# Kernel tuning notes

Hardware: AMD Instinct MI355X
Metric: run time of the kernel (lower is better)

## Reference

```python
import jax, jax.numpy as jnp
import numpy as np

NB_VARS = 2_000_000
N0 = 2 + 2 * NB_VARS      # input vector length: [zero, one, pos0, neg0, pos1, neg1, ...]
M0 = 4_000_000            # prod layer 0 outputs (binary fan-in)
M1 = 1_000_000            # sum  layer 1 outputs (irregular fan-in)
M2 = 500_000              # prod layer 2 outputs (binary fan-in)
M3 = 125_000              # sum  layer 3 outputs (irregular fan-in)


def setup_inputs() -> dict:
    key = jax.random.key(0)
    ks = jax.random.split(key, 7)
    x_pos = jax.random.uniform(ks[0], (NB_VARS,), dtype=jnp.float32)
    ix_in0 = jax.random.randint(ks[1], (2 * M0,), 0, N0)            # edges of prod layer 0
    ix_in1 = jax.random.randint(ks[2], (8_000_000,), 0, M0)         # edges of sum layer 1
    ix_out1 = jnp.sort(jax.random.randint(ks[3], (8_000_000,), 0, M1))
    ix_in2 = jax.random.randint(ks[4], (2 * M2,), 0, M1)            # edges of prod layer 2
    ix_in3 = jax.random.randint(ks[5], (1_000_000,), 0, M2)         # edges of sum layer 3
    ix_out3 = jnp.sort(jax.random.randint(ks[6], (1_000_000,), 0, M3))
    return {"x_pos": x_pos, "ix_in0": ix_in0, "ix_in1": ix_in1, "ix_out1": ix_out1,
            "ix_in2": ix_in2, "ix_in3": ix_in3, "ix_out3": ix_out3}


def reference(x_pos, ix_in0, ix_in1, ix_out1, ix_in2, ix_in3, ix_out3):
    # encode_input (real semiring): neg = negate(pos) = 1 - pos; interleave; prepend [zero=0, one=1]
    neg = 1.0 - x_pos
    units = jnp.array([0.0, 1.0], dtype=x_pos.dtype)
    x = jnp.concatenate([units, jnp.stack([x_pos, neg], axis=1).reshape(-1)])  # [N0]

    # layer 0: product layer, binary fan-in -> gather + pairwise multiply
    e0 = x[ix_in0].reshape(M0, 2)
    x = e0[:, 0] * e0[:, 1]                                                    # [M0]

    # layer 1: sum layer, irregular fan-in -> gather + segment-sum
    x = jax.ops.segment_sum(x[ix_in1], ix_out1, num_segments=M1)               # [M1]

    # layer 2: product layer, binary fan-in
    e2 = x[ix_in2].reshape(M2, 2)
    x = e2[:, 0] * e2[:, 1]                                                    # [M2]

    # layer 3: sum layer, irregular fan-in
    x = jax.ops.segment_sum(x[ix_in3], ix_out3, num_segments=M3)               # [M3]
    return x
```

## Files before the change

kernel.cpp:

```cpp
#include <hip/hip_runtime.h>
#include <hip/hip_fp16.h>


#define PERS_BLOCKS 2048
#define PERS_THREADS 256
#define WBITS_H 20

typedef __attribute__((ext_vector_type(4))) int   iv4;
typedef __attribute__((ext_vector_type(4))) float fv4;
typedef __attribute__((ext_vector_type(4))) unsigned int uv4;

__device__ __forceinline__ iv4 nt_load4(const int* p) {
    return __builtin_nontemporal_load((const iv4*)p);
}

__global__ void init_kernel(const float* __restrict__ in, unsigned int* __restrict__ x16,
                            float* __restrict__ y1, float* __restrict__ out,
                            int n4, int nz1, int nzo) {
    int t = blockIdx.x * blockDim.x + threadIdx.x;
    if (t < n4) {
        fv4 f = __builtin_nontemporal_load((const fv4*)(in + 4 * (size_t)t));
        __half2 lo = __floats2half2_rn(f.x, f.y);
        __half2 hi = __floats2half2_rn(f.z, f.w);
        unsigned int rlo = *(const unsigned int*)&lo;
        unsigned int rhi = *(const unsigned int*)&hi;
        x16[2 * t]     = rlo;
        x16[2 * t + 1] = rhi;
    }
    if (t < nz1) {
        fv4 z = {0.f, 0.f, 0.f, 0.f};
        __builtin_nontemporal_store(z, (fv4*)(y1 + 4 * (size_t)t));
    }
    if (t < nzo) {
        fv4 z = {0.f, 0.f, 0.f, 0.f};
        __builtin_nontemporal_store(z, (fv4*)(out + 4 * (size_t)t));
    }
}

__device__ __forceinline__ float decode16(const __half* __restrict__ xp, int idx) {
    int k = (idx - 2) >> 1;
    k = k < 0 ? 0 : k;
    float v = __half2float(xp[k]);
    v = (idx & 1) ? 1.0f - v : v;
    if (idx < 2) v = (float)idx;
    return v;
}

__global__ void layer0_prod8_kernel(const __half* __restrict__ x16,
                                    const int* __restrict__ ix,
                                    unsigned int* __restrict__ out16, int nT) {
    int t = blockIdx.x * blockDim.x + threadIdx.x;
    if (t >= nT) return;
    iv4 p0 = nt_load4(ix + 16 * (size_t)t);
    iv4 p1 = nt_load4(ix + 16 * (size_t)t + 4);
    iv4 p2 = nt_load4(ix + 16 * (size_t)t + 8);
    iv4 p3 = nt_load4(ix + 16 * (size_t)t + 12);
    float a0 = decode16(x16, p0.x), b0 = decode16(x16, p0.y);
    float a1 = decode16(x16, p0.z), b1 = decode16(x16, p0.w);
    float a2 = decode16(x16, p1.x), b2 = decode16(x16, p1.y);
    float a3 = decode16(x16, p1.z), b3 = decode16(x16, p1.w);
    float a4 = decode16(x16, p2.x), b4 = decode16(x16, p2.y);
    float a5 = decode16(x16, p2.z), b5 = decode16(x16, p2.w);
    float a6 = decode16(x16, p3.x), b6 = decode16(x16, p3.y);
    float a7 = decode16(x16, p3.z), b7 = decode16(x16, p3.w);
    __half2 h0 = __floats2half2_rn(a0 * b0, a1 * b1);
    __half2 h1 = __floats2half2_rn(a2 * b2, a3 * b3);
    __half2 h2 = __floats2half2_rn(a4 * b4, a5 * b5);
    __half2 h3 = __floats2half2_rn(a6 * b6, a7 * b7);
    uv4 r;
    r.x = *(const unsigned int*)&h0;
    r.y = *(const unsigned int*)&h1;
    r.z = *(const unsigned int*)&h2;
    r.w = *(const unsigned int*)&h3;
    __builtin_nontemporal_store(r, (uv4*)(out16 + 4 * (size_t)t));
}

template<int NS, int NWIN>
__global__ __launch_bounds__(PERS_THREADS)
void sum_win_h_kernel(const __half* __restrict__ vin,
                      const int* __restrict__ ix_in,
                      const int* __restrict__ ix_out,
                      float* __restrict__ out, int nT4) {
    const int nTh  = gridDim.x * blockDim.x;
    const int gtid = blockIdx.x * blockDim.x + threadIdx.x;
    const int lane = threadIdx.x & 63;

    iv4    a[NS];
    iv4    sg[NS];
    float4 v[NS];
    bool   act[NS];
    #pragma unroll
    for (int s = 0; s < NS; ++s) {
        int t = s * nTh + gtid;
        act[s] = (t < nT4);
        if (act[s]) {
            a[s]  = nt_load4(ix_in  + 4 * (size_t)t);
            sg[s] = nt_load4(ix_out + 4 * (size_t)t);
        } else {
            a[s]  = (iv4){-1, -1, -1, -1};
            sg[s] = (iv4){-1, -1, -1, -1};
        }
        v[s] = make_float4(0.f, 0.f, 0.f, 0.f);
    }

    #pragma unroll
    for (int w = 0; w < NWIN; ++w) {
        #pragma unroll
        for (int s = 0; s < NS; ++s) {
            if ((a[s].x >> WBITS_H) == w) v[s].x = __half2float(vin[a[s].x]);
            if ((a[s].y >> WBITS_H) == w) v[s].y = __half2float(vin[a[s].y]);
            if ((a[s].z >> WBITS_H) == w) v[s].z = __half2float(vin[a[s].z]);
            if ((a[s].w >> WBITS_H) == w) v[s].w = __half2float(vin[a[s].w]);
        }
    }

    #pragma unroll
    for (int s = 0; s < NS; ++s) {
        int seg = -1; float val = 0.f;
        if (act[s]) {
            int cur = sg[s].x; float acc = v[s].x;
            if (sg[s].y == cur) acc += v[s].y; else { atomicAdd(&out[cur], acc); cur = sg[s].y; acc = v[s].y; }
            if (sg[s].z == cur) acc += v[s].z; else { atomicAdd(&out[cur], acc); cur = sg[s].z; acc = v[s].z; }
            if (sg[s].w == cur) acc += v[s].w; else { atomicAdd(&out[cur], acc); cur = sg[s].w; acc = v[s].w; }
            seg = cur; val = acc;
        }
        #pragma unroll
        for (int off = 1; off < 64; off <<= 1) {
            float vv = __shfl_up(val, off, 64);
            int   ss = __shfl_up(seg, off, 64);
            if (lane >= off && ss == seg) val += vv;
        }
        int seg_next = __shfl_down(seg, 1, 64);
        bool is_last = (lane == 63) || (seg_next != seg);
        if (act[s] && is_last) atomicAdd(&out[seg], val);
    }
}

__global__ void sum4_f32_kernel(const float* __restrict__ vin,
                                const int* __restrict__ ix_in,
                                const int* __restrict__ ix_out,
                                float* __restrict__ out, int nT4) {
    int t = blockIdx.x * blockDim.x + threadIdx.x;
    int lane = threadIdx.x & 63;
    int seg = -1; float val = 0.f;
    if (t < nT4) {
        iv4 a  = nt_load4(ix_in  + 4 * (size_t)t);
        iv4 sg = nt_load4(ix_out + 4 * (size_t)t);
        float v0 = vin[a.x], v1 = vin[a.y], v2 = vin[a.z], v3 = vin[a.w];
        int cur = sg.x; float acc = v0;
        if (sg.y == cur) acc += v1; else { atomicAdd(&out[cur], acc); cur = sg.y; acc = v1; }
        if (sg.z == cur) acc += v2; else { atomicAdd(&out[cur], acc); cur = sg.z; acc = v2; }
        if (sg.w == cur) acc += v3; else { atomicAdd(&out[cur], acc); cur = sg.w; acc = v3; }
        seg = cur; val = acc;
    }
    #pragma unroll
    for (int off = 1; off < 64; off <<= 1) {
        float vv = __shfl_up(val, off, 64);
        int   ss = __shfl_up(seg, off, 64);
        if (lane >= off && ss == seg) val += vv;
    }
    int seg_next = __shfl_down(seg, 1, 64);
    bool is_last = (lane == 63) || (seg_next != seg);
    if (t < nT4 && is_last) atomicAdd(&out[seg], val);
}

__global__ void prod2_kernel(const float* __restrict__ vin,
                             const int* __restrict__ ix,
                             float2* __restrict__ out, int nT) {
    int t = blockIdx.x * blockDim.x + threadIdx.x;
    if (t >= nT) return;
    iv4 p = nt_load4(ix + 4 * (size_t)t);
    float a0 = vin[p.x], b0 = vin[p.y];
    float a1 = vin[p.z], b1 = vin[p.w];
    float2 r; r.x = a0 * b0; r.y = a1 * b1;
    out[t] = r;
}

extern "C" void kernel_launch(void* const* d_in, const int* in_sizes, int n_in,
                              void* d_out, int out_size, void* d_ws, size_t ws_size,
                              hipStream_t stream) {
    const float* x_pos  = (const float*)d_in[0];
    const int*   ix_in0 = (const int*)d_in[1];
    const int*   ix_in1 = (const int*)d_in[2];
    const int*   ix_out1= (const int*)d_in[3];
    const int*   ix_in2 = (const int*)d_in[4];
    const int*   ix_in3 = (const int*)d_in[5];
    const int*   ix_out3= (const int*)d_in[6];
    float* out = (float*)d_out;

    const int NV = in_sizes[0];
    const int M0 = in_sizes[1] / 2;
    const int E1 = in_sizes[2];
    const int M1 = 1000000;
    const int M2 = in_sizes[4] / 2;
    const int E3 = in_sizes[5];
    const int M3 = out_size;

    char* ws = (char*)d_ws;
    __half* y0  = (__half*)(ws);
    float*  y1  = (float*)(ws + (size_t)8  * 1024 * 1024);
    float*  y2  = (float*)(ws + (size_t)12 * 1024 * 1024);
    __half* x16 = (__half*)(ws + (size_t)14 * 1024 * 1024);

    const int B = 256;

    int n4  = NV / 4;
    int nz1 = M1 / 4;
    int nzo = M3 / 4;
    init_kernel<<<(n4 + B - 1) / B, B, 0, stream>>>(
        x_pos, (unsigned int*)x16, y1, out, n4, nz1, nzo);

    int t0 = M0 / 8;
    layer0_prod8_kernel<<<(t0 + B - 1) / B, B, 0, stream>>>(
        x16, ix_in0, (unsigned int*)y0, t0);

    int t1 = E1 / 4;
    sum_win_h_kernel<4, 4><<<PERS_BLOCKS, PERS_THREADS, 0, stream>>>(
        y0, ix_in1, ix_out1, y1, t1);

    int t2 = M2 / 2;
    prod2_kernel<<<(t2 + B - 1) / B, B, 0, stream>>>(
        y1, ix_in2, (float2*)y2, t2);

    int t3 = E3 / 4;
    sum4_f32_kernel<<<(t3 + B - 1) / B, B, 0, stream>>>(
        y2, ix_in3, ix_out3, out, t3);
}
```

Measured before the change: 253.8 us.

## Replace atomics with plain stores for wave-interior segments; restructure layer0 striding

In both segment-sum kernels, a segment whose run lies entirely inside one wavefront is now written with a plain store instead of an atomicAdd. Shuffles of the neighbouring lanes' first and last segment IDs decide this, and any segment that might span a wave boundary still uses atomics. The goal is to cut atomic traffic to global memory. Layer 0 is also rewritten so each thread handles four strided pairs-of-pairs, which changes the load pattern from 64-byte per-thread chunks to coalesced 16-byte loads.

```diff
diff --git a/kernel.cpp b/kernel.cpp
--- a/kernel.cpp
+++ b/kernel.cpp
@@ -46,33 +46,30 @@
     return v;
 }
 
-__global__ void layer0_prod8_kernel(const __half* __restrict__ x16,
-                                    const int* __restrict__ ix,
-                                    unsigned int* __restrict__ out16, int nT) {
-    int t = blockIdx.x * blockDim.x + threadIdx.x;
-    if (t >= nT) return;
-    iv4 p0 = nt_load4(ix + 16 * (size_t)t);
-    iv4 p1 = nt_load4(ix + 16 * (size_t)t + 4);
-    iv4 p2 = nt_load4(ix + 16 * (size_t)t + 8);
-    iv4 p3 = nt_load4(ix + 16 * (size_t)t + 12);
-    float a0 = decode16(x16, p0.x), b0 = decode16(x16, p0.y);
-    float a1 = decode16(x16, p0.z), b1 = decode16(x16, p0.w);
-    float a2 = decode16(x16, p1.x), b2 = decode16(x16, p1.y);
-    float a3 = decode16(x16, p1.z), b3 = decode16(x16, p1.w);
-    float a4 = decode16(x16, p2.x), b4 = decode16(x16, p2.y);
-    float a5 = decode16(x16, p2.z), b5 = decode16(x16, p2.w);
-    float a6 = decode16(x16, p3.x), b6 = decode16(x16, p3.y);
-    float a7 = decode16(x16, p3.z), b7 = decode16(x16, p3.w);
-    __half2 h0 = __floats2half2_rn(a0 * b0, a1 * b1);
-    __half2 h1 = __floats2half2_rn(a2 * b2, a3 * b3);
-    __half2 h2 = __floats2half2_rn(a4 * b4, a5 * b5);
-    __half2 h3 = __floats2half2_rn(a6 * b6, a7 * b7);
-    uv4 r;
-    r.x = *(const unsigned int*)&h0;
-    r.y = *(const unsigned int*)&h1;
-    r.z = *(const unsigned int*)&h2;
-    r.w = *(const unsigned int*)&h3;
-    __builtin_nontemporal_store(r, (uv4*)(out16 + 4 * (size_t)t));
+#define NS0 4
+__global__ void layer0_prod_kernel(const __half* __restrict__ x16,
+                                   const int* __restrict__ ix,
+                                   unsigned int* __restrict__ out16, int nQ) {
+    const int nTh  = gridDim.x * blockDim.x;
+    const int gtid = blockIdx.x * blockDim.x + threadIdx.x;
+    #pragma unroll
+    for (int s = 0; s < NS0; ++s) {
+        int t = s * nTh + gtid;
+        if (t < nQ) {
+            iv4 p = nt_load4(ix + 4 * (size_t)t);
+            float a0 = decode16(x16, p.x), b0 = decode16(x16, p.y);
+            float a1 = decode16(x16, p.z), b1 = decode16(x16, p.w);
+            __half2 h = __floats2half2_rn(a0 * b0, a1 * b1);
+            __builtin_nontemporal_store(*(const unsigned int*)&h, out16 + (size_t)t);
+        }
+    }
+}
+
+__device__ __forceinline__ void flush_run(float* __restrict__ out, int cur, float acc,
+                                          bool first, int lane, int prvw) {
+    bool plain = first ? (lane > 0 && prvw != cur) : true;
+    if (plain) out[cur] = acc;
+    else atomicAdd(&out[cur], acc);
 }
 
 template<int NS, int NWIN>
@@ -116,12 +113,22 @@
 
     #pragma unroll
     for (int s = 0; s < NS; ++s) {
+        int seg_first = __shfl(sg[s].x, 0, 64);
+        int prvw      = __shfl_up(sg[s].w, 1, 64);
+        int nxt_first = __shfl_down(sg[s].x, 1, 64);
+
         int seg = -1; float val = 0.f;
         if (act[s]) {
-            int cur = sg[s].x; float acc = v[s].x;
-            if (sg[s].y == cur) acc += v[s].y; else { atomicAdd(&out[cur], acc); cur = sg[s].y; acc = v[s].y; }
-            if (sg[s].z == cur) acc += v[s].z; else { atomicAdd(&out[cur], acc); cur = sg[s].z; acc = v[s].z; }
-            if (sg[s].w == cur) acc += v[s].w; else { atomicAdd(&out[cur], acc); cur = sg[s].w; acc = v[s].w; }
+            int cur = sg[s].x; float acc = v[s].x; bool first = true;
+            if (sg[s].y == cur) acc += v[s].y;
+            else { flush_run(out, cur, acc, first, lane, prvw);
+                   cur = sg[s].y; acc = v[s].y; first = false; }
+            if (sg[s].z == cur) acc += v[s].z;
+            else { flush_run(out, cur, acc, first, lane, prvw);
+                   cur = sg[s].z; acc = v[s].z; first = false; }
+            if (sg[s].w == cur) acc += v[s].w;
+            else { flush_run(out, cur, acc, first, lane, prvw);
+                   cur = sg[s].w; acc = v[s].w; first = false; }
             seg = cur; val = acc;
         }
         #pragma unroll
@@ -132,7 +139,11 @@
         }
         int seg_next = __shfl_down(seg, 1, 64);
         bool is_last = (lane == 63) || (seg_next != seg);
-        if (act[s] && is_last) atomicAdd(&out[seg], val);
+        bool cont    = (lane == 63) || (nxt_first == seg);
+        if (act[s] && is_last) {
+            if (!cont && seg > seg_first) out[seg] = val;
+            else atomicAdd(&out[seg], val);
+        }
     }
 }
 
@@ -142,15 +153,32 @@
                                 float* __restrict__ out, int nT4) {
     int t = blockIdx.x * blockDim.x + threadIdx.x;
     int lane = threadIdx.x & 63;
+    bool act = (t < nT4);
+    iv4 a, sg;
+    if (act) {
+        a  = nt_load4(ix_in  + 4 * (size_t)t);
+        sg = nt_load4(ix_out + 4 * (size_t)t);
+    } else {
+        a  = (iv4){-1, -1, -1, -1};
+        sg = (iv4){-1, -1, -1, -1};
+    }
+    int seg_first = __shfl(sg.x, 0, 64);
+    int prvw      = __shfl_up(sg.w, 1, 64);
+    int nxt_first = __shfl_down(sg.x, 1, 64);
+
     int seg = -1; float val = 0.f;
-    if (t < nT4) {
-        iv4 a  = nt_load4(ix_in  + 4 * (size_t)t);
-        iv4 sg = nt_load4(ix_out + 4 * (size_t)t);
+    if (act) {
         float v0 = vin[a.x], v1 = vin[a.y], v2 = vin[a.z], v3 = vin[a.w];
-        int cur = sg.x; float acc = v0;
-        if (sg.y == cur) acc += v1; else { atomicAdd(&out[cur], acc); cur = sg.y; acc = v1; }
-        if (sg.z == cur) acc += v2; else { atomicAdd(&out[cur], acc); cur = sg.z; acc = v2; }
-        if (sg.w == cur) acc += v3; else { atomicAdd(&out[cur], acc); cur = sg.w; acc = v3; }
+        int cur = sg.x; float acc = v0; bool first = true;
+        if (sg.y == cur) acc += v1;
+        else { flush_run(out, cur, acc, first, lane, prvw);
+               cur = sg.y; acc = v1; first = false; }
+        if (sg.z == cur) acc += v2;
+        else { flush_run(out, cur, acc, first, lane, prvw);
+               cur = sg.z; acc = v2; first = false; }
+        if (sg.w == cur) acc += v3;
+        else { flush_run(out, cur, acc, first, lane, prvw);
+               cur = sg.w; acc = v3; first = false; }
         seg = cur; val = acc;
     }
     #pragma unroll
@@ -161,7 +189,11 @@
     }
     int seg_next = __shfl_down(seg, 1, 64);
     bool is_last = (lane == 63) || (seg_next != seg);
-    if (t < nT4 && is_last) atomicAdd(&out[seg], val);
+    bool cont    = (lane == 63) || (nxt_first == seg);
+    if (act && is_last) {
+        if (!cont && seg > seg_first) out[seg] = val;
+        else atomicAdd(&out[seg], val);
+    }
 }
 
 __global__ void prod2_kernel(const float* __restrict__ vin,
@@ -210,9 +242,10 @@
     init_kernel<<<(n4 + B - 1) / B, B, 0, stream>>>(
         x_pos, (unsigned int*)x16, y1, out, n4, nz1, nzo);
 
-    int t0 = M0 / 8;
-    layer0_prod8_kernel<<<(t0 + B - 1) / B, B, 0, stream>>>(
-        x16, ix_in0, (unsigned int*)y0, t0);
+    int nQ = M0 / 2;
+    int g0 = (nQ + NS0 * B - 1) / (NS0 * B);
+    layer0_prod_kernel<<<g0, B, 0, stream>>>(
+        x16, ix_in0, (unsigned int*)y0, nQ);
 
     int t1 = E1 / 4;
     sum_win_h_kernel<4, 4><<<PERS_BLOCKS, PERS_THREADS, 0, stream>>>(
```

Measured after the change: 282.2 us. +11.2%, slower.

## Replace windowed persistent layer-1 gather with simple one-pass grid kernel

Applied to the files above, without the earlier changes.

Removes the persistent kernel that split the fp16 gather into four address windows, with four work items per thread, to keep each window cache-resident. Uses a plain one-thread-per-4-edges kernel over the whole grid, gathering all four values directly before the segmented reduction. This drops the windowing loop and its per-window compare overhead and raises parallelism, but gives up the L2 locality the windows were meant to provide for the 8 MB fp16 source.

```diff
diff --git a/kernel.cpp b/kernel.cpp
--- a/kernel.cpp
+++ b/kernel.cpp
@@ -1,10 +1,6 @@
 #include <hip/hip_runtime.h>
 #include <hip/hip_fp16.h>
 
-
-#define PERS_BLOCKS 2048
-#define PERS_THREADS 256
-#define WBITS_H 20
 
 typedef __attribute__((ext_vector_type(4))) int   iv4;
 typedef __attribute__((ext_vector_type(4))) float fv4;
@@ -75,65 +71,35 @@
     __builtin_nontemporal_store(r, (uv4*)(out16 + 4 * (size_t)t));
 }
 
-template<int NS, int NWIN>
-__global__ __launch_bounds__(PERS_THREADS)
-void sum_win_h_kernel(const __half* __restrict__ vin,
-                      const int* __restrict__ ix_in,
-                      const int* __restrict__ ix_out,
-                      float* __restrict__ out, int nT4) {
-    const int nTh  = gridDim.x * blockDim.x;
-    const int gtid = blockIdx.x * blockDim.x + threadIdx.x;
-    const int lane = threadIdx.x & 63;
-
-    iv4    a[NS];
-    iv4    sg[NS];
-    float4 v[NS];
-    bool   act[NS];
+__global__ void sum4_h_kernel(const __half* __restrict__ vin,
+                              const int* __restrict__ ix_in,
+                              const int* __restrict__ ix_out,
+                              float* __restrict__ out, int nT4) {
+    int t = blockIdx.x * blockDim.x + threadIdx.x;
+    int lane = threadIdx.x & 63;
+    int seg = -1; float val = 0.f;
+    if (t < nT4) {
+        iv4 a  = nt_load4(ix_in  + 4 * (size_t)t);
+        iv4 sg = nt_load4(ix_out + 4 * (size_t)t);
+        float v0 = __half2float(vin[a.x]);
+        float v1 = __half2float(vin[a.y]);
+        float v2 = __half2float(vin[a.z]);
+        float v3 = __half2float(vin[a.w]);
+        int cur = sg.x; float acc = v0;
+        if (sg.y == cur) acc += v1; else { atomicAdd(&out[cur], acc); cur = sg.y; acc = v1; }
+        if (sg.z == cur) acc += v2; else { atomicAdd(&out[cur], acc); cur = sg.z; acc = v2; }
+        if (sg.w == cur) acc += v3; else { atomicAdd(&out[cur], acc); cur = sg.w; acc = v3; }
+        seg = cur; val = acc;
+    }
     #pragma unroll
-    for (int s = 0; s < NS; ++s) {
-        int t = s * nTh + gtid;
-        act[s] = (t < nT4);
-        if (act[s]) {
-            a[s]  = nt_load4(ix_in  + 4 * (size_t)t);
-            sg[s] = nt_load4(ix_out + 4 * (size_t)t);
-        } else {
-            a[s]  = (iv4){-1, -1, -1, -1};
-            sg[s] = (iv4){-1, -1, -1, -1};
-        }
-        v[s] = make_float4(0.f, 0.f, 0.f, 0.f);
+    for (int off = 1; off < 64; off <<= 1) {
+        float vv = __shfl_up(val, off, 64);
+        int   ss = __shfl_up(seg, off, 64);
+        if (lane >= off && ss == seg) val += vv;
     }
-
-    #pragma unroll
-    for (int w = 0; w < NWIN; ++w) {
-        #pragma unroll
-        for (int s = 0; s < NS; ++s) {
-            if ((a[s].x >> WBITS_H) == w) v[s].x = __half2float(vin[a[s].x]);
-            if ((a[s].y >> WBITS_H) == w) v[s].y = __half2float(vin[a[s].y]);
-            if ((a[s].z >> WBITS_H) == w) v[s].z = __half2float(vin[a[s].z]);
-            if ((a[s].w >> WBITS_H) == w) v[s].w = __half2float(vin[a[s].w]);
-        }
-    }
-
-    #pragma unroll
-    for (int s = 0; s < NS; ++s) {
-        int seg = -1; float val = 0.f;
-        if (act[s]) {
-            int cur = sg[s].x; float acc = v[s].x;
-            if (sg[s].y == cur) acc += v[s].y; else { atomicAdd(&out[cur], acc); cur = sg[s].y; acc = v[s].y; }
-            if (sg[s].z == cur) acc += v[s].z; else { atomicAdd(&out[cur], acc); cur = sg[s].z; acc = v[s].z; }
-            if (sg[s].w == cur) acc += v[s].w; else { atomicAdd(&out[cur], acc); cur = sg[s].w; acc = v[s].w; }
-            seg = cur; val = acc;
-        }
-        #pragma unroll
-        for (int off = 1; off < 64; off <<= 1) {
-            float vv = __shfl_up(val, off, 64);
-            int   ss = __shfl_up(seg, off, 64);
-            if (lane >= off && ss == seg) val += vv;
-        }
-        int seg_next = __shfl_down(seg, 1, 64);
-        bool is_last = (lane == 63) || (seg_next != seg);
-        if (act[s] && is_last) atomicAdd(&out[seg], val);
-    }
+    int seg_next = __shfl_down(seg, 1, 64);
+    bool is_last = (lane == 63) || (seg_next != seg);
+    if (t < nT4 && is_last) atomicAdd(&out[seg], val);
 }
 
 __global__ void sum4_f32_kernel(const float* __restrict__ vin,
@@ -215,7 +181,7 @@
         x16, ix_in0, (unsigned int*)y0, t0);
 
     int t1 = E1 / 4;
-    sum_win_h_kernel<4, 4><<<PERS_BLOCKS, PERS_THREADS, 0, stream>>>(
+    sum4_h_kernel<<<(t1 + B - 1) / B, B, 0, stream>>>(
         y0, ix_in1, ix_out1, y1, t1);
 
     int t2 = M2 / 2;
```

New measurement: 266.2 us. 4.9% more time.

## Fuse input encoding and zeroing into layer 0, fold layer-2 product into layer 3

Applied to the files above, without the earlier changes.

Removes the separate init kernel by decoding fp32 inputs directly in the layer-0 gather and zeroing the accumulation buffers there. Removes the layer-2 product kernel by having the layer-3 segment-sum gather the index pair and multiply on the fly. This cuts two launches and the intermediate buffer traffic. In exchange, layer 3 does redundant gathers for reused nodes, and the layer-0 gather reads a larger fp32 table with worse cache locality.

```diff
diff --git a/kernel.cpp b/kernel.cpp
--- a/kernel.cpp
+++ b/kernel.cpp
@@ -14,55 +14,43 @@
     return __builtin_nontemporal_load((const iv4*)p);
 }
 
-__global__ void init_kernel(const float* __restrict__ in, unsigned int* __restrict__ x16,
-                            float* __restrict__ y1, float* __restrict__ out,
-                            int n4, int nz1, int nzo) {
+__device__ __forceinline__ float decode32(const float* __restrict__ xp, int idx) {
+    int k = (idx - 2) >> 1;
+    k = k < 0 ? 0 : k;
+    float v = xp[k];
+    v = (idx & 1) ? 1.0f - v : v;
+    if (idx < 2) v = (float)idx;
+    return v;
+}
+
+__global__ void layer0_prod8_zero_kernel(const float* __restrict__ xp,
+                                         const int* __restrict__ ix,
+                                         unsigned int* __restrict__ out16,
+                                         float* __restrict__ y1,
+                                         float* __restrict__ outv,
+                                         int nT, int nz1, int nzo) {
     int t = blockIdx.x * blockDim.x + threadIdx.x;
-    if (t < n4) {
-        fv4 f = __builtin_nontemporal_load((const fv4*)(in + 4 * (size_t)t));
-        __half2 lo = __floats2half2_rn(f.x, f.y);
-        __half2 hi = __floats2half2_rn(f.z, f.w);
-        unsigned int rlo = *(const unsigned int*)&lo;
-        unsigned int rhi = *(const unsigned int*)&hi;
-        x16[2 * t]     = rlo;
-        x16[2 * t + 1] = rhi;
-    }
     if (t < nz1) {
         fv4 z = {0.f, 0.f, 0.f, 0.f};
         __builtin_nontemporal_store(z, (fv4*)(y1 + 4 * (size_t)t));
     }
     if (t < nzo) {
         fv4 z = {0.f, 0.f, 0.f, 0.f};
-        __builtin_nontemporal_store(z, (fv4*)(out + 4 * (size_t)t));
-    }
-}
-
-__device__ __forceinline__ float decode16(const __half* __restrict__ xp, int idx) {
-    int k = (idx - 2) >> 1;
-    k = k < 0 ? 0 : k;
-    float v = __half2float(xp[k]);
-    v = (idx & 1) ? 1.0f - v : v;
-    if (idx < 2) v = (float)idx;
-    return v;
-}
-
-__global__ void layer0_prod8_kernel(const __half* __restrict__ x16,
-                                    const int* __restrict__ ix,
-                                    unsigned int* __restrict__ out16, int nT) {
-    int t = blockIdx.x * blockDim.x + threadIdx.x;
+        __builtin_nontemporal_store(z, (fv4*)(outv + 4 * (size_t)t));
+    }
     if (t >= nT) return;
     iv4 p0 = nt_load4(ix + 16 * (size_t)t);
     iv4 p1 = nt_load4(ix + 16 * (size_t)t + 4);
     iv4 p2 = nt_load4(ix + 16 * (size_t)t + 8);
     iv4 p3 = nt_load4(ix + 16 * (size_t)t + 12);
-    float a0 = decode16(x16, p0.x), b0 = decode16(x16, p0.y);
-    float a1 = decode16(x16, p0.z), b1 = decode16(x16, p0.w);
-    float a2 = decode16(x16, p1.x), b2 = decode16(x16, p1.y);
-    float a3 = decode16(x16, p1.z), b3 = decode16(x16, p1.w);
-    float a4 = decode16(x16, p2.x), b4 = decode16(x16, p2.y);
-    float a5 = decode16(x16, p2.z), b5 = decode16(x16, p2.w);
-    float a6 = decode16(x16, p3.x), b6 = decode16(x16, p3.y);
-    float a7 = decode16(x16, p3.z), b7 = decode16(x16, p3.w);
+    float a0 = decode32(xp, p0.x), b0 = decode32(xp, p0.y);
+    float a1 = decode32(xp, p0.z), b1 = decode32(xp, p0.w);
+    float a2 = decode32(xp, p1.x), b2 = decode32(xp, p1.y);
+    float a3 = decode32(xp, p1.z), b3 = decode32(xp, p1.w);
+    float a4 = decode32(xp, p2.x), b4 = decode32(xp, p2.y);
+    float a5 = decode32(xp, p2.z), b5 = decode32(xp, p2.w);
+    float a6 = decode32(xp, p3.x), b6 = decode32(xp, p3.y);
+    float a7 = decode32(xp, p3.z), b7 = decode32(xp, p3.w);
     __half2 h0 = __floats2half2_rn(a0 * b0, a1 * b1);
     __half2 h1 = __floats2half2_rn(a2 * b2, a3 * b3);
     __half2 h2 = __floats2half2_rn(a4 * b4, a5 * b5);
@@ -136,17 +124,25 @@
     }
 }
 
-__global__ void sum4_f32_kernel(const float* __restrict__ vin,
-                                const int* __restrict__ ix_in,
-                                const int* __restrict__ ix_out,
-                                float* __restrict__ out, int nT4) {
+__global__ void sum4_prod_f32_kernel(const float* __restrict__ y1,
+                                     const int* __restrict__ ix2,
+                                     const int* __restrict__ ix_in3,
+                                     const int* __restrict__ ix_out3,
+                                     float* __restrict__ out, int nT4) {
     int t = blockIdx.x * blockDim.x + threadIdx.x;
     int lane = threadIdx.x & 63;
     int seg = -1; float val = 0.f;
     if (t < nT4) {
-        iv4 a  = nt_load4(ix_in  + 4 * (size_t)t);
-        iv4 sg = nt_load4(ix_out + 4 * (size_t)t);
-        float v0 = vin[a.x], v1 = vin[a.y], v2 = vin[a.z], v3 = vin[a.w];
+        iv4 a  = nt_load4(ix_in3  + 4 * (size_t)t);
+        iv4 sg = nt_load4(ix_out3 + 4 * (size_t)t);
+        int2 q0 = *(const int2*)(ix2 + 2 * (size_t)a.x);
+        int2 q1 = *(const int2*)(ix2 + 2 * (size_t)a.y);
+        int2 q2 = *(const int2*)(ix2 + 2 * (size_t)a.z);
+        int2 q3 = *(const int2*)(ix2 + 2 * (size_t)a.w);
+        float v0 = y1[q0.x] * y1[q0.y];
+        float v1 = y1[q1.x] * y1[q1.y];
+        float v2 = y1[q2.x] * y1[q2.y];
+        float v3 = y1[q3.x] * y1[q3.y];
         int cur = sg.x; float acc = v0;
         if (sg.y == cur) acc += v1; else { atomicAdd(&out[cur], acc); cur = sg.y; acc = v1; }
         if (sg.z == cur) acc += v2; else { atomicAdd(&out[cur], acc); cur = sg.z; acc = v2; }
@@ -162,18 +158,6 @@
     int seg_next = __shfl_down(seg, 1, 64);
     bool is_last = (lane == 63) || (seg_next != seg);
     if (t < nT4 && is_last) atomicAdd(&out[seg], val);
-}
-
-__global__ void prod2_kernel(const float* __restrict__ vin,
-                             const int* __restrict__ ix,
-                             float2* __restrict__ out, int nT) {
-    int t = blockIdx.x * blockDim.x + threadIdx.x;
-    if (t >= nT) return;
-    iv4 p = nt_load4(ix + 4 * (size_t)t);
-    float a0 = vin[p.x], b0 = vin[p.y];
-    float a1 = vin[p.z], b1 = vin[p.w];
-    float2 r; r.x = a0 * b0; r.y = a1 * b1;
-    out[t] = r;
 }
 
 extern "C" void kernel_launch(void* const* d_in, const int* in_sizes, int n_in,
@@ -188,41 +172,29 @@
     const int*   ix_out3= (const int*)d_in[6];
     float* out = (float*)d_out;
 
-    const int NV = in_sizes[0];
     const int M0 = in_sizes[1] / 2;
     const int E1 = in_sizes[2];
     const int M1 = 1000000;
-    const int M2 = in_sizes[4] / 2;
     const int E3 = in_sizes[5];
     const int M3 = out_size;
 
     char* ws = (char*)d_ws;
-    __half* y0  = (__half*)(ws);
-    float*  y1  = (float*)(ws + (size_t)8  * 1024 * 1024);
-    float*  y2  = (float*)(ws + (size_t)12 * 1024 * 1024);
-    __half* x16 = (__half*)(ws + (size_t)14 * 1024 * 1024);
+    __half* y0 = (__half*)(ws);
+    float*  y1 = (float*)(ws + (size_t)8 * 1024 * 1024);
 
     const int B = 256;
 
-    int n4  = NV / 4;
+    int t0  = M0 / 8;
     int nz1 = M1 / 4;
     int nzo = M3 / 4;
-    init_kernel<<<(n4 + B - 1) / B, B, 0, stream>>>(
-        x_pos, (unsigned int*)x16, y1, out, n4, nz1, nzo);
-
-    int t0 = M0 / 8;
-    layer0_prod8_kernel<<<(t0 + B - 1) / B, B, 0, stream>>>(
-        x16, ix_in0, (unsigned int*)y0, t0);
+    layer0_prod8_zero_kernel<<<(t0 + B - 1) / B, B, 0, stream>>>(
+        x_pos, ix_in0, (unsigned int*)y0, y1, out, t0, nz1, nzo);
 
     int t1 = E1 / 4;
     sum_win_h_kernel<4, 4><<<PERS_BLOCKS, PERS_THREADS, 0, stream>>>(
         y0, ix_in1, ix_out1, y1, t1);
 
-    int t2 = M2 / 2;
-    prod2_kernel<<<(t2 + B - 1) / B, B, 0, stream>>>(
-        y1, ix_in2, (float2*)y2, t2);
-
     int t3 = E3 / 4;
-    sum4_f32_kernel<<<(t3 + B - 1) / B, B, 0, stream>>>(
-        y2, ix_in3, ix_out3, out, t3);
-}
+    sum4_prod_f32_kernel<<<(t3 + B - 1) / B, B, 0, stream>>>(
+        y1, ix_in2, ix_in3, ix_out3, out, t3);
+}
```

Result: slower. 287.6 us (+13.3%).
